# Kernel optimization log

Hardware: AMD Instinct MI355X
Metric: run time of the kernel (lower is better)

Reference implementation:

```python
import jax, jax.numpy as jnp
import numpy as np

D_MODEL = 1024
NUM_HEADS = 16
DFF = 4096
DEPTH = D_MODEL // NUM_HEADS
EPS = 1e-6


def setup_inputs() -> dict:
    key = jax.random.key(0)
    ks = jax.random.split(key, 12)
    B, S, D = 4, 2048, D_MODEL
    scale = 0.02
    inp = {
        "x": jax.random.normal(ks[0], (B, S, D), dtype=jnp.float32),
        "mask": jnp.zeros((B, 1, 1, S), dtype=jnp.float32),
        "wq": jax.random.normal(ks[1], (D, D), dtype=jnp.float32) * scale,
        "bq": jnp.zeros((D,), dtype=jnp.float32),
        "wk": jax.random.normal(ks[2], (D, D), dtype=jnp.float32) * scale,
        "bk": jnp.zeros((D,), dtype=jnp.float32),
        "wv": jax.random.normal(ks[3], (D, D), dtype=jnp.float32) * scale,
        "bv": jnp.zeros((D,), dtype=jnp.float32),
        "wo": jax.random.normal(ks[4], (D, D), dtype=jnp.float32) * scale,
        "bo": jnp.zeros((D,), dtype=jnp.float32),
        "w1": jax.random.normal(ks[5], (D, DFF), dtype=jnp.float32) * scale,
        "b1": jnp.zeros((DFF,), dtype=jnp.float32),
        "w2": jax.random.normal(ks[6], (DFF, D), dtype=jnp.float32) * scale,
        "b2": jnp.zeros((D,), dtype=jnp.float32),
        "g1": jnp.ones((D,), dtype=jnp.float32),
        "beta1": jnp.zeros((D,), dtype=jnp.float32),
        "g2": jnp.ones((D,), dtype=jnp.float32),
        "beta2": jnp.zeros((D,), dtype=jnp.float32),
    }
    return inp


def _layernorm(x, gamma, beta):
    mu = jnp.mean(x, axis=-1, keepdims=True)
    var = jnp.mean(jnp.square(x - mu), axis=-1, keepdims=True)
    return (x - mu) * jax.lax.rsqrt(var + EPS) * gamma + beta


def _split_heads(t, B, S):
    # [B,S,D] -> [B,H,S,depth]
    return t.reshape(B, S, NUM_HEADS, DEPTH).transpose(0, 2, 1, 3)


def encoder_layer(x, mask, wq, bq, wk, bk, wv, bv, wo, bo,
                  w1, b1, w2, b2, g1, beta1, g2, beta2):
    B, S, D = x.shape
    q = _split_heads(x @ wq + bq, B, S)
    k = _split_heads(x @ wk + bk, B, S)
    v = _split_heads(x @ wv + bv, B, S)
    logits = jnp.einsum("bhqd,bhkd->bhqk", q, k) / jnp.sqrt(
        jnp.asarray(DEPTH, dtype=x.dtype))
    if mask is not None:
        logits = logits + mask * -1e9
    attn = jax.nn.softmax(logits, axis=-1)
    ctx = jnp.einsum("bhqk,bhkd->bhqd", attn, v)
    ctx = ctx.transpose(0, 2, 1, 3).reshape(B, S, D)
    attn_out = ctx @ wo + bo
    out1 = _layernorm(x + attn_out, g1, beta1)
    ffn = jax.nn.relu(out1 @ w1 + b1) @ w2 + b2
    out2 = _layernorm(out1 + ffn, g2, beta2)
    return out2


def reference(x, mask, wq, bq, wk, bk, wv, bv, wo, bo,
              w1, b1, w2, b2, g1, beta1, g2, beta2):
    return encoder_layer(x, mask, wq, bq, wk, bk, wv, bv, wo, bo,
                         w1, b1, w2, b2, g1, beta1, g2, beta2)
```

## Files before the change

### kernel.cpp

```cpp
#include <hip/hip_runtime.h>
#include <cstdint>


#define BATCH 4
#define SEQ   2048
#define DM    1024
#define NH    16
#define DEPTH 64
#define DFF_  4096
#define EPSF  1e-6f

typedef short bf16x8 __attribute__((ext_vector_type(8)));
typedef float f32x4  __attribute__((ext_vector_type(4)));

__device__ __forceinline__ unsigned short f2bf(float f) {
  union { float f; unsigned int u; } v; v.f = f;
  unsigned int u = v.u;
  return (unsigned short)((u + 0x7fffu + ((u >> 16) & 1u)) >> 16);
}

__device__ __forceinline__ void gload_lds16(const void* g, void* l) {
  __builtin_amdgcn_global_load_lds(
      (const __attribute__((address_space(1))) unsigned int*)g,
      (__attribute__((address_space(3))) unsigned int*)l, 16, 0, 0);
}

#define VMCNT(n) asm volatile("s_waitcnt vmcnt(" #n ")" ::: "memory")

template<int EPI>
__global__ __launch_bounds__(512, 2)
void gemm8(const unsigned short* __restrict__ A, const unsigned short* __restrict__ Bt,
           const float* __restrict__ bias0, const float* __restrict__ bias1,
           const float* __restrict__ bias2, float* __restrict__ Cf,
           unsigned short* __restrict__ Cb0, unsigned short* __restrict__ Cb1,
           unsigned short* __restrict__ Cb2, int M, int N, int K)
{
  __shared__ char smem[131072];
  const int tid  = threadIdx.x;
  const int lane = tid & 63;
  const int wid  = tid >> 6;
  const int wr   = wid >> 2;
  const int wcn  = wid & 3;
  const int fr   = lane & 15;
  const int kh   = lane >> 4;

  const int nbx  = N >> 8;
  const int nwg  = gridDim.x;
  const int flat = blockIdx.x;
  const int swz  = (flat & 7) * (nwg >> 3) + (flat >> 3);
  const int bx = swz % nbx, by = swz / nbx;
  const int m0 = by << 8, n0 = bx << 8;

  const int lr  = tid >> 3;
  const int ch  = tid & 7;
  const int sch = ch ^ (lr & 7);
  const char* gA = (const char*)A + ((size_t)(m0 + lr) * K) * 2 + sch * 16;
  const char* gB = (const char*)Bt + ((size_t)(n0 + lr) * K) * 2 + sch * 16;
  const size_t rstep = (size_t)K * 128;

  const int chk0 = ((kh) ^ (fr & 7)) * 16;
  const int chk1 = ((4 + kh) ^ (fr & 7)) * 16;
  const int rowA = wr * 128 + fr;
  const int rowB = wcn * 64 + fr;

  f32x4 acc[8][4] = {};
  bf16x8 bg[4][2];
  const int NT = K >> 6;

  {
    char* sb = smem;
    gload_lds16(gB + 0 * rstep, sb + 32768 + 0 * 8192 + tid * 16);
    gload_lds16(gB + 1 * rstep, sb + 32768 + 1 * 8192 + tid * 16);
    gload_lds16(gB + 2 * rstep, sb + 32768 + 2 * 8192 + tid * 16);
    gload_lds16(gB + 3 * rstep, sb + 32768 + 3 * 8192 + tid * 16);
    gload_lds16(gA + 0 * rstep, sb + 0 * 8192 + tid * 16);
    gload_lds16(gA + 2 * rstep, sb + 2 * 8192 + tid * 16);
    gload_lds16(gA + 1 * rstep, sb + 1 * 8192 + tid * 16);
    gload_lds16(gA + 3 * rstep, sb + 3 * 8192 + tid * 16);
    VMCNT(2);
    __builtin_amdgcn_s_barrier();
  }

  for (int t = 0; t < NT - 1; ++t) {
    char* rb = smem + ((t & 1) << 16);
    char* sb = smem + (((t + 1) & 1) << 16);
    const size_t kg = (size_t)(t + 1) * 128;
#pragma unroll
    for (int p = 0; p < 4; ++p) {
      if (p == 0) {
        gload_lds16(gB + kg + 0 * rstep, sb + 32768 + 0 * 8192 + tid * 16);
        gload_lds16(gB + kg + 1 * rstep, sb + 32768 + 1 * 8192 + tid * 16);
      } else if (p == 1) {
        gload_lds16(gB + kg + 2 * rstep, sb + 32768 + 2 * 8192 + tid * 16);
        gload_lds16(gB + kg + 3 * rstep, sb + 32768 + 3 * 8192 + tid * 16);
      } else if (p == 2) {
        gload_lds16(gA + kg + 0 * rstep, sb + 0 * 8192 + tid * 16);
        gload_lds16(gA + kg + 2 * rstep, sb + 2 * 8192 + tid * 16);
      } else {
        gload_lds16(gA + kg + 1 * rstep, sb + 1 * 8192 + tid * 16);
        gload_lds16(gA + kg + 3 * rstep, sb + 3 * 8192 + tid * 16);
      }
      if (p == 0) {
#pragma unroll
        for (int j = 0; j < 4; ++j) {
          bg[j][0] = *(const bf16x8*)(rb + 32768 + (rowB + j * 16) * 128 + chk0);
          bg[j][1] = *(const bf16x8*)(rb + 32768 + (rowB + j * 16) * 128 + chk1);
        }
      }
      bf16x8 a00 = *(const bf16x8*)(rb + (rowA + (2 * p) * 16) * 128 + chk0);
      bf16x8 a01 = *(const bf16x8*)(rb + (rowA + (2 * p) * 16) * 128 + chk1);
      bf16x8 a10 = *(const bf16x8*)(rb + (rowA + (2 * p + 1) * 16) * 128 + chk0);
      bf16x8 a11 = *(const bf16x8*)(rb + (rowA + (2 * p + 1) * 16) * 128 + chk1);
      __builtin_amdgcn_s_barrier();
      __builtin_amdgcn_s_setprio(1);
#pragma unroll
      for (int j = 0; j < 4; ++j) {
        acc[2*p][j]   = __builtin_amdgcn_mfma_f32_16x16x32_bf16(a00, bg[j][0], acc[2*p][j], 0, 0, 0);
        acc[2*p][j]   = __builtin_amdgcn_mfma_f32_16x16x32_bf16(a01, bg[j][1], acc[2*p][j], 0, 0, 0);
        acc[2*p+1][j] = __builtin_amdgcn_mfma_f32_16x16x32_bf16(a10, bg[j][0], acc[2*p+1][j], 0, 0, 0);
        acc[2*p+1][j] = __builtin_amdgcn_mfma_f32_16x16x32_bf16(a11, bg[j][1], acc[2*p+1][j], 0, 0, 0);
      }
      __builtin_amdgcn_s_setprio(0);
      if (p == 1) VMCNT(4);
      if (p == 3) VMCNT(2);
      __builtin_amdgcn_s_barrier();
    }
  }
  {
    char* rb = smem + (((NT - 1) & 1) << 16);
#pragma unroll
    for (int p = 0; p < 4; ++p) {
      if (p == 0) {
#pragma unroll
        for (int j = 0; j < 4; ++j) {
          bg[j][0] = *(const bf16x8*)(rb + 32768 + (rowB + j * 16) * 128 + chk0);
          bg[j][1] = *(const bf16x8*)(rb + 32768 + (rowB + j * 16) * 128 + chk1);
        }
      }
      bf16x8 a00 = *(const bf16x8*)(rb + (rowA + (2 * p) * 16) * 128 + chk0);
      bf16x8 a01 = *(const bf16x8*)(rb + (rowA + (2 * p) * 16) * 128 + chk1);
      bf16x8 a10 = *(const bf16x8*)(rb + (rowA + (2 * p + 1) * 16) * 128 + chk0);
      bf16x8 a11 = *(const bf16x8*)(rb + (rowA + (2 * p + 1) * 16) * 128 + chk1);
      __builtin_amdgcn_s_barrier();
      __builtin_amdgcn_s_setprio(1);
#pragma unroll
      for (int j = 0; j < 4; ++j) {
        acc[2*p][j]   = __builtin_amdgcn_mfma_f32_16x16x32_bf16(a00, bg[j][0], acc[2*p][j], 0, 0, 0);
        acc[2*p][j]   = __builtin_amdgcn_mfma_f32_16x16x32_bf16(a01, bg[j][1], acc[2*p][j], 0, 0, 0);
        acc[2*p+1][j] = __builtin_amdgcn_mfma_f32_16x16x32_bf16(a10, bg[j][0], acc[2*p+1][j], 0, 0, 0);
        acc[2*p+1][j] = __builtin_amdgcn_mfma_f32_16x16x32_bf16(a11, bg[j][1], acc[2*p+1][j], 0, 0, 0);
      }
      __builtin_amdgcn_s_setprio(0);
      if (p == 1) VMCNT(0);
      __builtin_amdgcn_s_barrier();
    }
  }

  if (EPI == 2) {
    const int seg = n0 >> 10;
    const float* bp = seg == 0 ? bias0 : (seg == 1 ? bias1 : bias2);
    unsigned short* dst = seg == 0 ? Cb0 : (seg == 1 ? Cb1 : Cb2);
    float bc[4];
#pragma unroll
    for (int j = 0; j < 4; ++j) bc[j] = bp[(n0 & 1023) + wcn * 64 + j * 16 + fr];
#pragma unroll
    for (int m = 0; m < 8; ++m)
#pragma unroll
      for (int jj = 0; jj < 4; ++jj) {
        const int row = m0 + wr * 128 + m * 16 + kh * 4 + jj;
        const int b = row >> 11, s = row & (SEQ - 1);
#pragma unroll
        for (int j = 0; j < 4; ++j) {
          const int cs = (n0 & 1023) + wcn * 64 + j * 16 + fr;
          const int hh = cs >> 6, d = cs & 63;
          const float v = acc[m][j][jj] + bc[j];
          if (seg < 2)
            dst[(((size_t)(b * NH + hh)) * SEQ + s) * DEPTH + d] = f2bf(v);
          else
            dst[(((size_t)(b * NH + hh)) * DEPTH + d) * SEQ + s] = f2bf(v);
        }
      }
  } else {
    float bc[4];
#pragma unroll
    for (int j = 0; j < 4; ++j) bc[j] = bias0[n0 + wcn * 64 + j * 16 + fr];
#pragma unroll
    for (int m = 0; m < 8; ++m)
#pragma unroll
      for (int jj = 0; jj < 4; ++jj) {
        const int row = m0 + wr * 128 + m * 16 + kh * 4 + jj;
#pragma unroll
        for (int j = 0; j < 4; ++j) {
          const int col = n0 + wcn * 64 + j * 16 + fr;
          float v = acc[m][j][jj] + bc[j];
          if (EPI == 1) {
            v = fmaxf(v, 0.f);
            Cb0[(size_t)row * N + col] = f2bf(v);
          } else {
            Cf[(size_t)row * N + col] = v;
          }
        }
      }
  }
}

__global__ __launch_bounds__(256)
void transpose_to_bf16(const float* __restrict__ W, unsigned short* __restrict__ Wt,
                       int K, int N)
{
  __shared__ float t[32][33];
  const int tx = threadIdx.x & 31;
  const int ty = threadIdx.x >> 5;
  const int n0 = blockIdx.x * 32;
  const int k0 = blockIdx.y * 32;
#pragma unroll
  for (int i = 0; i < 4; ++i) {
    int r = ty + i * 8;
    t[r][tx] = W[(size_t)(k0 + r) * N + n0 + tx];
  }
  __syncthreads();
#pragma unroll
  for (int i = 0; i < 4; ++i) {
    int r = ty + i * 8;
    Wt[(size_t)(n0 + r) * K + k0 + tx] = f2bf(t[tx][r]);
  }
}

__global__ __launch_bounds__(256)
void convert_bf16(const float* __restrict__ X, unsigned short* __restrict__ Xb, int n4)
{
  int i = blockIdx.x * 256 + threadIdx.x;
  if (i < n4) {
    float4 v = ((const float4*)X)[i];
    ushort4 r;
    r.x = f2bf(v.x); r.y = f2bf(v.y); r.z = f2bf(v.z); r.w = f2bf(v.w);
    ((ushort4*)Xb)[i] = r;
  }
}

__global__ __launch_bounds__(256)
void attn_mfma(const unsigned short* __restrict__ Qb, const unsigned short* __restrict__ Kb,
               const unsigned short* __restrict__ Vtb, const float* __restrict__ mask,
               unsigned short* __restrict__ ctxb)
{
  __shared__ unsigned short Ks[64 * 64];
  __shared__ unsigned short Vts[64 * 64];
  __shared__ unsigned short Ps[4][16 * 72];
  __shared__ float Ms[SEQ];

  const int tid  = threadIdx.x;
  const int w    = tid >> 6;
  const int lane = tid & 63;
  const int fr   = lane & 15;
  const int kh   = lane >> 4;
  const int rbase = kh * 4;
  const int bh = blockIdx.y;
  const int b  = bh >> 4, hh = bh & 15;
  const int q0 = blockIdx.x * 64;

  for (int i = tid; i < SEQ / 4; i += 256)
    *(float4*)&Ms[i * 4] = *(const float4*)&mask[(size_t)b * SEQ + i * 4];

  const size_t qrow = ((size_t)bh * SEQ + q0 + w * 16 + fr) * DEPTH;
  bf16x8 bq[2];
  bq[0] = *(const bf16x8*)(Qb + qrow + kh * 8);
  bq[1] = *(const bf16x8*)(Qb + qrow + 32 + kh * 8);

  float m_run = -1e30f, l_run = 0.f;
  f32x4 o[4] = {};

  const int stg_chunk = (lane & 7) ^ (lane >> 3);
  const int r8 = lane >> 3;
  unsigned short* Pw = &Ps[w][0];

  for (int kv0 = 0; kv0 < SEQ; kv0 += 64) {
    __syncthreads();
#pragma unroll
    for (int i = 0; i < 2; ++i) {
      int rr = w * 16 + i * 8 + r8;
      gload_lds16((const char*)Kb + (((size_t)bh * SEQ + kv0 + rr) * DEPTH) * 2 + stg_chunk * 16,
                  (char*)Ks + (w * 16 + i * 8) * 128);
      gload_lds16((const char*)Vtb + (((size_t)bh * DEPTH + rr) * SEQ + kv0) * 2 + stg_chunk * 16,
                  (char*)Vts + (w * 16 + i * 8) * 128);
    }
    __syncthreads();

    f32x4 s[4] = {};
#pragma unroll
    for (int ks = 0; ks < 2; ++ks)
#pragma unroll
      for (int j = 0; j < 4; ++j) {
        bf16x8 ak = *(const bf16x8*)((const char*)Ks + (j * 16 + fr) * 128 +
                                     (((ks * 4 + kh) ^ (fr & 7)) * 16));
        s[j] = __builtin_amdgcn_mfma_f32_16x16x32_bf16(ak, bq[ks], s[j], 0, 0, 0);
      }

    float p[16];
    float pmax = -1e30f;
#pragma unroll
    for (int j = 0; j < 4; ++j) {
      float4 mk = *(const float4*)&Ms[kv0 + j * 16 + rbase];
#pragma unroll
      for (int jj = 0; jj < 4; ++jj) {
        float vsc = s[j][jj] * 0.125f + ((const float*)&mk)[jj] * (-1e9f);
        p[j * 4 + jj] = vsc;
        pmax = fmaxf(pmax, vsc);
      }
    }
    pmax = fmaxf(pmax, __shfl_xor(pmax, 16));
    pmax = fmaxf(pmax, __shfl_xor(pmax, 32));
    float mnew = fmaxf(m_run, pmax);
    float sc = __expf(m_run - mnew);
    float rs = 0.f;
#pragma unroll
    for (int t = 0; t < 16; ++t) { p[t] = __expf(p[t] - mnew); rs += p[t]; }
    rs += __shfl_xor(rs, 16);
    rs += __shfl_xor(rs, 32);
    l_run = l_run * sc + rs;
    m_run = mnew;
#pragma unroll
    for (int db = 0; db < 4; ++db) {
      o[db][0] *= sc; o[db][1] *= sc; o[db][2] *= sc; o[db][3] *= sc;
    }

#pragma unroll
    for (int j = 0; j < 4; ++j) {
      unsigned int lo = (unsigned)f2bf(p[j * 4 + 0]) | ((unsigned)f2bf(p[j * 4 + 1]) << 16);
      unsigned int hi = (unsigned)f2bf(p[j * 4 + 2]) | ((unsigned)f2bf(p[j * 4 + 3]) << 16);
      unsigned long long pk = (unsigned long long)lo | ((unsigned long long)hi << 32);
      *(unsigned long long*)((char*)Pw + fr * 144 + (j * 16 + rbase) * 2) = pk;
    }
#pragma unroll
    for (int ks = 0; ks < 2; ++ks) {
      bf16x8 bp = *(const bf16x8*)((char*)Pw + fr * 144 + ks * 64 + kh * 16);
#pragma unroll
      for (int db = 0; db < 4; ++db) {
        bf16x8 av = *(const bf16x8*)((const char*)Vts + (db * 16 + fr) * 128 +
                                     (((ks * 4 + kh) ^ (fr & 7)) * 16));
        o[db] = __builtin_amdgcn_mfma_f32_16x16x32_bf16(av, bp, o[db], 0, 0, 0);
      }
    }
  }

  float inv = 1.f / l_run;
  const int srow = q0 + w * 16 + fr;
#pragma unroll
  for (int db = 0; db < 4; ++db) {
    ushort4 rb;
    rb.x = f2bf(o[db][0] * inv); rb.y = f2bf(o[db][1] * inv);
    rb.z = f2bf(o[db][2] * inv); rb.w = f2bf(o[db][3] * inv);
    *(ushort4*)(ctxb + ((size_t)(b * SEQ + srow)) * DM + hh * 64 + db * 16 + rbase) = rb;
  }
}

template<int DUAL>
__global__ __launch_bounds__(256)
void add_ln_kernel(const float* __restrict__ X, const float* __restrict__ Y,
                   const float* __restrict__ g, const float* __restrict__ be,
                   float* __restrict__ out, unsigned short* __restrict__ outb)
{
  __shared__ float red[8];
  const int row = blockIdx.x;
  const int tid = threadIdx.x;
  const size_t off = (size_t)row * DM + tid * 4;
  float4 xv = *(const float4*)(X + off);
  float4 yv = *(const float4*)(Y + off);
  float v0 = xv.x + yv.x, v1 = xv.y + yv.y, v2 = xv.z + yv.z, v3 = xv.w + yv.w;
  float s = v0 + v1 + v2 + v3;
#pragma unroll
  for (int m = 1; m < 64; m <<= 1) s += __shfl_xor(s, m);
  if ((tid & 63) == 0) red[tid >> 6] = s;
  __syncthreads();
  float mean = (red[0] + red[1] + red[2] + red[3]) * (1.f / DM);
  float d0 = v0 - mean, d1 = v1 - mean, d2 = v2 - mean, d3 = v3 - mean;
  float sq = d0 * d0 + d1 * d1 + d2 * d2 + d3 * d3;
#pragma unroll
  for (int m = 1; m < 64; m <<= 1) sq += __shfl_xor(sq, m);
  if ((tid & 63) == 0) red[4 + (tid >> 6)] = sq;
  __syncthreads();
  float var = (red[4] + red[5] + red[6] + red[7]) * (1.f / DM);
  float inv = rsqrtf(var + EPSF);
  int col = tid * 4;
  float4 r;
  r.x = d0 * inv * g[col + 0] + be[col + 0];
  r.y = d1 * inv * g[col + 1] + be[col + 1];
  r.z = d2 * inv * g[col + 2] + be[col + 2];
  r.w = d3 * inv * g[col + 3] + be[col + 3];
  *(float4*)(out + off) = r;
  if (DUAL) {
    ushort4 rb;
    rb.x = f2bf(r.x); rb.y = f2bf(r.y); rb.z = f2bf(r.z); rb.w = f2bf(r.w);
    *(ushort4*)(outb + off) = rb;
  }
}

extern "C" void kernel_launch(void* const* d_in, const int* in_sizes, int n_in,
                              void* d_out, int out_size, void* d_ws, size_t ws_size,
                              hipStream_t stream)
{
  const float* x    = (const float*)d_in[0];
  const float* mask = (const float*)d_in[1];
  const float* wq   = (const float*)d_in[2];
  const float* bq   = (const float*)d_in[3];
  const float* wk   = (const float*)d_in[4];
  const float* bk   = (const float*)d_in[5];
  const float* wv   = (const float*)d_in[6];
  const float* bv   = (const float*)d_in[7];
  const float* wo   = (const float*)d_in[8];
  const float* bo   = (const float*)d_in[9];
  const float* w1   = (const float*)d_in[10];
  const float* b1   = (const float*)d_in[11];
  const float* w2   = (const float*)d_in[12];
  const float* b2   = (const float*)d_in[13];
  const float* g1   = (const float*)d_in[14];
  const float* be1  = (const float*)d_in[15];
  const float* g2   = (const float*)d_in[16];
  const float* be2  = (const float*)d_in[17];
  float* out = (float*)d_out;
  char* wsb = (char*)d_ws;

  unsigned short* qb    = (unsigned short*)(wsb);
  unsigned short* kb    = (unsigned short*)(wsb + (16u << 20));
  unsigned short* vtb   = (unsigned short*)(wsb + (32u << 20));
  unsigned short* ctxb  = (unsigned short*)(wsb + (48u << 20));
  unsigned short* xb    = (unsigned short*)(wsb + (64u << 20));
  unsigned short* hbuf  = (unsigned short*)(wsb + (80u << 20));
  unsigned short* wqkvt = (unsigned short*)(wsb + (144u << 20));
  unsigned short* wot   = (unsigned short*)(wsb + (150u << 20));
  unsigned short* w1t   = (unsigned short*)(wsb + (152u << 20));
  unsigned short* w2t   = (unsigned short*)(wsb + (160u << 20));
  float* attn_out = (float*)(wsb);
  float* out1     = (float*)(wsb + (32u << 20));
  unsigned short* out1b = xb;
  float* ffn      = (float*)(wsb);

  dim3 blk(256);
  const int M = BATCH * SEQ;

  convert_bf16<<<8192, blk, 0, stream>>>(x, xb, (BATCH * SEQ * DM) / 4);
  transpose_to_bf16<<<dim3(32, 32), blk, 0, stream>>>(wq, wqkvt, DM, DM);
  transpose_to_bf16<<<dim3(32, 32), blk, 0, stream>>>(wk, wqkvt + 1024 * 1024, DM, DM);
  transpose_to_bf16<<<dim3(32, 32), blk, 0, stream>>>(wv, wqkvt + 2 * 1024 * 1024, DM, DM);
  transpose_to_bf16<<<dim3(32, 32), blk, 0, stream>>>(wo, wot, DM, DM);
  transpose_to_bf16<<<dim3(128, 32), blk, 0, stream>>>(w1, w1t, DM, DFF_);
  transpose_to_bf16<<<dim3(32, 128), blk, 0, stream>>>(w2, w2t, DFF_, DM);

  gemm8<2><<<dim3((M / 256) * (3072 / 256)), dim3(512), 0, stream>>>(
      xb, wqkvt, bq, bk, bv, nullptr, qb, kb, vtb, M, 3072, DM);

  attn_mfma<<<dim3(SEQ / 64, BATCH * NH), blk, 0, stream>>>(qb, kb, vtb, mask, ctxb);

  gemm8<0><<<dim3((M / 256) * (DM / 256)), dim3(512), 0, stream>>>(
      ctxb, wot, bo, nullptr, nullptr, attn_out, nullptr, nullptr, nullptr, M, DM, DM);
  add_ln_kernel<1><<<dim3(M), blk, 0, stream>>>(x, attn_out, g1, be1, out1, out1b);

  gemm8<1><<<dim3((M / 256) * (DFF_ / 256)), dim3(512), 0, stream>>>(
      out1b, w1t, b1, nullptr, nullptr, nullptr, hbuf, nullptr, nullptr, M, DFF_, DM);
  gemm8<0><<<dim3((M / 256) * (DM / 256)), dim3(512), 0, stream>>>(
      hbuf, w2t, b2, nullptr, nullptr, ffn, nullptr, nullptr, nullptr, M, DM, DFF_);

  add_ln_kernel<0><<<dim3(M), blk, 0, stream>>>(out1, ffn, g2, be2, out, nullptr);
}
```

Before: 636.4 us.

## Add 128x256 GEMM kernel, double-buffer attention K/V, use exp2 softmax

New measurement: 639.4 us. About the same (+0.5%).

```diff
diff --git a/kernel.cpp b/kernel.cpp
--- a/kernel.cpp
+++ b/kernel.cpp
@@ -204,6 +204,169 @@
   }
 }
 
+template<int EPI>
+__global__ __launch_bounds__(512, 2)
+void gemm128(const unsigned short* __restrict__ A, const unsigned short* __restrict__ Bt,
+             const float* __restrict__ bias0, const float* __restrict__ bias1,
+             const float* __restrict__ bias2, float* __restrict__ Cf,
+             unsigned short* __restrict__ Cb0, unsigned short* __restrict__ Cb1,
+             unsigned short* __restrict__ Cb2, int M, int N, int K)
+{
+  __shared__ char smem[98304];
+  const int tid  = threadIdx.x;
+  const int lane = tid & 63;
+  const int wid  = tid >> 6;
+  const int fr   = lane & 15;
+  const int kh   = lane >> 4;
+
+  const int nbx  = N >> 8;
+  const int nwg  = gridDim.x;
+  const int flat = blockIdx.x;
+  const int swz  = (flat & 7) * (nwg >> 3) + (flat >> 3);
+  const int bx = swz % nbx, by = swz / nbx;
+  const int m0 = by << 7, n0 = bx << 8;
+
+  const int lr  = tid >> 3;
+  const int sch = (tid & 7) ^ (lr & 7);
+  const char* gA = (const char*)A + ((size_t)(m0 + lr) * K) * 2 + sch * 16;
+  const char* gB = (const char*)Bt + ((size_t)(n0 + lr) * K) * 2 + sch * 16;
+  const size_t rstep = (size_t)K * 128;
+
+  const int chk0 = ((kh) ^ (fr & 7)) * 16;
+  const int chk1 = ((4 + kh) ^ (fr & 7)) * 16;
+  const int rowB = wid * 32 + fr;
+
+  f32x4 acc[8][2] = {};
+  bf16x8 bg[2][2];
+  const int NT = K >> 6;
+
+  {
+    char* sb = smem;
+    gload_lds16(gB + 0 * rstep, sb + 16384 + 0 * 8192 + tid * 16);
+    gload_lds16(gB + 1 * rstep, sb + 16384 + 1 * 8192 + tid * 16);
+    gload_lds16(gB + 2 * rstep, sb + 16384 + 2 * 8192 + tid * 16);
+    gload_lds16(gB + 3 * rstep, sb + 16384 + 3 * 8192 + tid * 16);
+    gload_lds16(gA + 0 * rstep, sb + 0 * 8192 + tid * 16);
+    gload_lds16(gA + 1 * rstep, sb + 1 * 8192 + tid * 16);
+    VMCNT(1);
+    __builtin_amdgcn_s_barrier();
+  }
+
+  for (int t = 0; t < NT - 1; ++t) {
+    char* rb = smem + (t & 1) * 49152;
+    char* sb = smem + ((t + 1) & 1) * 49152;
+    const size_t kg = (size_t)(t + 1) * 128;
+#pragma unroll
+    for (int p = 0; p < 4; ++p) {
+      if (p == 0) {
+        gload_lds16(gB + kg + 0 * rstep, sb + 16384 + 0 * 8192 + tid * 16);
+        gload_lds16(gB + kg + 1 * rstep, sb + 16384 + 1 * 8192 + tid * 16);
+      } else if (p == 1) {
+        gload_lds16(gB + kg + 2 * rstep, sb + 16384 + 2 * 8192 + tid * 16);
+        gload_lds16(gB + kg + 3 * rstep, sb + 16384 + 3 * 8192 + tid * 16);
+      } else if (p == 2) {
+        gload_lds16(gA + kg + 0 * rstep, sb + 0 * 8192 + tid * 16);
+      } else {
+        gload_lds16(gA + kg + 1 * rstep, sb + 1 * 8192 + tid * 16);
+      }
+      if (p == 0) {
+#pragma unroll
+        for (int j = 0; j < 2; ++j) {
+          bg[j][0] = *(const bf16x8*)(rb + 16384 + (rowB + j * 16) * 128 + chk0);
+          bg[j][1] = *(const bf16x8*)(rb + 16384 + (rowB + j * 16) * 128 + chk1);
+        }
+      }
+      bf16x8 a00 = *(const bf16x8*)(rb + ((2 * p) * 16 + fr) * 128 + chk0);
+      bf16x8 a01 = *(const bf16x8*)(rb + ((2 * p) * 16 + fr) * 128 + chk1);
+      bf16x8 a10 = *(const bf16x8*)(rb + ((2 * p + 1) * 16 + fr) * 128 + chk0);
+      bf16x8 a11 = *(const bf16x8*)(rb + ((2 * p + 1) * 16 + fr) * 128 + chk1);
+      __builtin_amdgcn_s_barrier();
+      __builtin_amdgcn_s_setprio(1);
+#pragma unroll
+      for (int j = 0; j < 2; ++j) {
+        acc[2*p][j]   = __builtin_amdgcn_mfma_f32_16x16x32_bf16(a00, bg[j][0], acc[2*p][j], 0, 0, 0);
+        acc[2*p][j]   = __builtin_amdgcn_mfma_f32_16x16x32_bf16(a01, bg[j][1], acc[2*p][j], 0, 0, 0);
+        acc[2*p+1][j] = __builtin_amdgcn_mfma_f32_16x16x32_bf16(a10, bg[j][0], acc[2*p+1][j], 0, 0, 0);
+        acc[2*p+1][j] = __builtin_amdgcn_mfma_f32_16x16x32_bf16(a11, bg[j][1], acc[2*p+1][j], 0, 0, 0);
+      }
+      __builtin_amdgcn_s_setprio(0);
+      if (p == 1) VMCNT(4);
+      if (p == 3) VMCNT(1);
+      __builtin_amdgcn_s_barrier();
+    }
+  }
+  {
+    char* rb = smem + ((NT - 1) & 1) * 49152;
+#pragma unroll
+    for (int p = 0; p < 4; ++p) {
+      if (p == 0) {
+#pragma unroll
+        for (int j = 0; j < 2; ++j) {
+          bg[j][0] = *(const bf16x8*)(rb + 16384 + (rowB + j * 16) * 128 + chk0);
+          bg[j][1] = *(const bf16x8*)(rb + 16384 + (rowB + j * 16) * 128 + chk1);
+        }
+      }
+      bf16x8 a00 = *(const bf16x8*)(rb + ((2 * p) * 16 + fr) * 128 + chk0);
+      bf16x8 a01 = *(const bf16x8*)(rb + ((2 * p) * 16 + fr) * 128 + chk1);
+      bf16x8 a10 = *(const bf16x8*)(rb + ((2 * p + 1) * 16 + fr) * 128 + chk0);
+      bf16x8 a11 = *(const bf16x8*)(rb + ((2 * p + 1) * 16 + fr) * 128 + chk1);
+      __builtin_amdgcn_s_barrier();
+      __builtin_amdgcn_s_setprio(1);
+#pragma unroll
+      for (int j = 0; j < 2; ++j) {
+        acc[2*p][j]   = __builtin_amdgcn_mfma_f32_16x16x32_bf16(a00, bg[j][0], acc[2*p][j], 0, 0, 0);
+        acc[2*p][j]   = __builtin_amdgcn_mfma_f32_16x16x32_bf16(a01, bg[j][1], acc[2*p][j], 0, 0, 0);
+        acc[2*p+1][j] = __builtin_amdgcn_mfma_f32_16x16x32_bf16(a10, bg[j][0], acc[2*p+1][j], 0, 0, 0);
+        acc[2*p+1][j] = __builtin_amdgcn_mfma_f32_16x16x32_bf16(a11, bg[j][1], acc[2*p+1][j], 0, 0, 0);
+      }
+      __builtin_amdgcn_s_setprio(0);
+      if (p == 1) VMCNT(0);
+      __builtin_amdgcn_s_barrier();
+    }
+  }
+
+  if (EPI == 2) {
+    const int seg = n0 >> 10;
+    const float* bp = seg == 0 ? bias0 : (seg == 1 ? bias1 : bias2);
+    unsigned short* dst = seg == 0 ? Cb0 : (seg == 1 ? Cb1 : Cb2);
+    float bc[2];
+#pragma unroll
+    for (int j = 0; j < 2; ++j) bc[j] = bp[(n0 & 1023) + wid * 32 + j * 16 + fr];
+#pragma unroll
+    for (int m = 0; m < 8; ++m)
+#pragma unroll
+      for (int jj = 0; jj < 4; ++jj) {
+        const int row = m0 + m * 16 + kh * 4 + jj;
+        const int b = row >> 11, s = row & (SEQ - 1);
+#pragma unroll
+        for (int j = 0; j < 2; ++j) {
+          const int cs = (n0 & 1023) + wid * 32 + j * 16 + fr;
+          const int hh = cs >> 6, d = cs & 63;
+          const float v = acc[m][j][jj] + bc[j];
+          if (seg < 2)
+            dst[(((size_t)(b * NH + hh)) * SEQ + s) * DEPTH + d] = f2bf(v);
+          else
+            dst[(((size_t)(b * NH + hh)) * DEPTH + d) * SEQ + s] = f2bf(v);
+        }
+      }
+  } else {
+    float bc[2];
+#pragma unroll
+    for (int j = 0; j < 2; ++j) bc[j] = bias0[n0 + wid * 32 + j * 16 + fr];
+#pragma unroll
+    for (int m = 0; m < 8; ++m)
+#pragma unroll
+      for (int jj = 0; jj < 4; ++jj) {
+        const int row = m0 + m * 16 + kh * 4 + jj;
+#pragma unroll
+        for (int j = 0; j < 2; ++j) {
+          const int col = n0 + wid * 32 + j * 16 + fr;
+          Cf[(size_t)row * N + col] = acc[m][j][jj] + bc[j];
+        }
+      }
+  }
+}
+
 __global__ __launch_bounds__(256)
 void transpose_to_bf16(const float* __restrict__ W, unsigned short* __restrict__ Wt,
                        int K, int N)
@@ -243,8 +406,8 @@
                const unsigned short* __restrict__ Vtb, const float* __restrict__ mask,
                unsigned short* __restrict__ ctxb)
 {
-  __shared__ unsigned short Ks[64 * 64];
-  __shared__ unsigned short Vts[64 * 64];
+  __shared__ unsigned short Ks[2][64 * 64];
+  __shared__ unsigned short Vts[2][64 * 64];
   __shared__ unsigned short Ps[4][16 * 72];
   __shared__ float Ms[SEQ];
 
@@ -258,8 +421,14 @@
   const int b  = bh >> 4, hh = bh & 15;
   const int q0 = blockIdx.x * 64;
 
-  for (int i = tid; i < SEQ / 4; i += 256)
-    *(float4*)&Ms[i * 4] = *(const float4*)&mask[(size_t)b * SEQ + i * 4];
+  const float MSCL = -1.0e9f * 1.44269504f;
+  const float SSCL = 0.125f * 1.44269504f;
+
+  for (int i = tid; i < SEQ / 4; i += 256) {
+    float4 mv = *(const float4*)&mask[(size_t)b * SEQ + i * 4];
+    mv.x *= MSCL; mv.y *= MSCL; mv.z *= MSCL; mv.w *= MSCL;
+    *(float4*)&Ms[i * 4] = mv;
+  }
 
   const size_t qrow = ((size_t)bh * SEQ + q0 + w * 16 + fr) * DEPTH;
   bf16x8 bq[2];
@@ -273,24 +442,33 @@
   const int r8 = lane >> 3;
   unsigned short* Pw = &Ps[w][0];
 
-  for (int kv0 = 0; kv0 < SEQ; kv0 += 64) {
-    __syncthreads();
+  auto stage = [&](int buf, int kv) {
 #pragma unroll
     for (int i = 0; i < 2; ++i) {
       int rr = w * 16 + i * 8 + r8;
-      gload_lds16((const char*)Kb + (((size_t)bh * SEQ + kv0 + rr) * DEPTH) * 2 + stg_chunk * 16,
-                  (char*)Ks + (w * 16 + i * 8) * 128);
-      gload_lds16((const char*)Vtb + (((size_t)bh * DEPTH + rr) * SEQ + kv0) * 2 + stg_chunk * 16,
-                  (char*)Vts + (w * 16 + i * 8) * 128);
-    }
-    __syncthreads();
+      gload_lds16((const char*)Kb + (((size_t)bh * SEQ + kv + rr) * DEPTH) * 2 + stg_chunk * 16,
+                  (char*)&Ks[buf][0] + (w * 16 + i * 8) * 128);
+      gload_lds16((const char*)Vtb + (((size_t)bh * DEPTH + rr) * SEQ + kv) * 2 + stg_chunk * 16,
+                  (char*)&Vts[buf][0] + (w * 16 + i * 8) * 128);
+    }
+  };
+
+  stage(0, 0);
+  __syncthreads();
+
+  int cur = 0;
+  for (int kv0 = 0; kv0 < SEQ; kv0 += 64) {
+    if (kv0 + 64 < SEQ) stage(cur ^ 1, kv0 + 64);
+
+    const char* kb_ = (const char*)&Ks[cur][0];
+    const char* vb_ = (const char*)&Vts[cur][0];
 
     f32x4 s[4] = {};
 #pragma unroll
     for (int ks = 0; ks < 2; ++ks)
 #pragma unroll
       for (int j = 0; j < 4; ++j) {
-        bf16x8 ak = *(const bf16x8*)((const char*)Ks + (j * 16 + fr) * 128 +
+        bf16x8 ak = *(const bf16x8*)(kb_ + (j * 16 + fr) * 128 +
                                      (((ks * 4 + kh) ^ (fr & 7)) * 16));
         s[j] = __builtin_amdgcn_mfma_f32_16x16x32_bf16(ak, bq[ks], s[j], 0, 0, 0);
       }
@@ -302,7 +480,7 @@
       float4 mk = *(const float4*)&Ms[kv0 + j * 16 + rbase];
 #pragma unroll
       for (int jj = 0; jj < 4; ++jj) {
-        float vsc = s[j][jj] * 0.125f + ((const float*)&mk)[jj] * (-1e9f);
+        float vsc = fmaf(s[j][jj], SSCL, ((const float*)&mk)[jj]);
         p[j * 4 + jj] = vsc;
         pmax = fmaxf(pmax, vsc);
       }
@@ -310,10 +488,10 @@
     pmax = fmaxf(pmax, __shfl_xor(pmax, 16));
     pmax = fmaxf(pmax, __shfl_xor(pmax, 32));
     float mnew = fmaxf(m_run, pmax);
-    float sc = __expf(m_run - mnew);
+    float sc = exp2f(m_run - mnew);
     float rs = 0.f;
 #pragma unroll
-    for (int t = 0; t < 16; ++t) { p[t] = __expf(p[t] - mnew); rs += p[t]; }
+    for (int t = 0; t < 16; ++t) { p[t] = exp2f(p[t] - mnew); rs += p[t]; }
     rs += __shfl_xor(rs, 16);
     rs += __shfl_xor(rs, 32);
     l_run = l_run * sc + rs;
@@ -335,11 +513,15 @@
       bf16x8 bp = *(const bf16x8*)((char*)Pw + fr * 144 + ks * 64 + kh * 16);
 #pragma unroll
       for (int db = 0; db < 4; ++db) {
-        bf16x8 av = *(const bf16x8*)((const char*)Vts + (db * 16 + fr) * 128 +
+        bf16x8 av = *(const bf16x8*)(vb_ + (db * 16 + fr) * 128 +
                                      (((ks * 4 + kh) ^ (fr & 7)) * 16));
         o[db] = __builtin_amdgcn_mfma_f32_16x16x32_bf16(av, bp, o[db], 0, 0, 0);
       }
     }
+
+    VMCNT(0);
+    __builtin_amdgcn_s_barrier();
+    cur ^= 1;
   }
 
   float inv = 1.f / l_run;
@@ -445,18 +627,18 @@
   transpose_to_bf16<<<dim3(128, 32), blk, 0, stream>>>(w1, w1t, DM, DFF_);
   transpose_to_bf16<<<dim3(32, 128), blk, 0, stream>>>(w2, w2t, DFF_, DM);
 
-  gemm8<2><<<dim3((M / 256) * (3072 / 256)), dim3(512), 0, stream>>>(
+  gemm128<2><<<dim3((M / 128) * (3072 / 256)), dim3(512), 0, stream>>>(
       xb, wqkvt, bq, bk, bv, nullptr, qb, kb, vtb, M, 3072, DM);
 
   attn_mfma<<<dim3(SEQ / 64, BATCH * NH), blk, 0, stream>>>(qb, kb, vtb, mask, ctxb);
 
-  gemm8<0><<<dim3((M / 256) * (DM / 256)), dim3(512), 0, stream>>>(
+  gemm128<0><<<dim3((M / 128) * (DM / 256)), dim3(512), 0, stream>>>(
       ctxb, wot, bo, nullptr, nullptr, attn_out, nullptr, nullptr, nullptr, M, DM, DM);
   add_ln_kernel<1><<<dim3(M), blk, 0, stream>>>(x, attn_out, g1, be1, out1, out1b);
 
   gemm8<1><<<dim3((M / 256) * (DFF_ / 256)), dim3(512), 0, stream>>>(
       out1b, w1t, b1, nullptr, nullptr, nullptr, hbuf, nullptr, nullptr, M, DFF_, DM);
-  gemm8<0><<<dim3((M / 256) * (DM / 256)), dim3(512), 0, stream>>>(
+  gemm128<0><<<dim3((M / 128) * (DM / 256)), dim3(512), 0, stream>>>(
       hbuf, w2t, b2, nullptr, nullptr, ffn, nullptr, nullptr, nullptr, M, DM, DFF_);
 
   add_ln_kernel<0><<<dim3(M), blk, 0, stream>>>(out1, ffn, g2, be2, out, nullptr);
```
